# Kernel tuning notes

Hardware: AMD Instinct MI355X
Metric: run time of the kernel (lower is better)

The kernel has to match this reference:

```python
import jax, jax.numpy as jnp
import numpy as np

ALPHA = 1.0   # alpha=1 -> loss = alpha*loss_shape; temporal term weighted by (1-alpha)=0
GAMMA = 0.01  # soft-DTW smoothing
G = 0.05      # logistic weight steepness (weighted-DTW, Jeong et al. 2011)
BIG = 1e9     # finite 'infinity' (keeps vjp NaN-free vs. true inf)


def _softdtw(D, gamma):
    # Soft-DTW value of cost matrix D [N,N] via anti-diagonal (wavefront) scan.
    # R(i,j) = D[i,j] + softmin_gamma(R(i-1,j-1), R(i-1,j), R(i,j-1)),
    # R(-1,-1)=0, other out-of-range = +inf. Diagonal k holds cells (i, k-i).
    N = D.shape[-1]
    i = jnp.arange(N)

    def step(carry, k):
        r2, r1 = carry            # diagonals k-2 and k-1, indexed by row i
        j = k - i
        valid = (j >= 0) & (j < N)
        dk = jnp.where(valid, D[i, jnp.clip(j, 0, N - 1)], 0.0)
        up = jnp.where(i > 0, jnp.roll(r1, 1), BIG)     # R(i-1, j)
        left = r1                                        # R(i, j-1) (BIG where invalid)
        dg = jnp.where(i > 0, jnp.roll(r2, 1), BIG)      # R(i-1, j-1)
        dg = jnp.where((i == 0) & (j == 0), 0.0, dg)     # R(-1,-1) = 0 boundary
        smin = -gamma * jax.nn.logsumexp(jnp.stack([-dg, -up, -left]) / gamma, axis=0)
        rk = jnp.where(valid, dk + smin, BIG)
        return (r1, rk), None

    r0 = jnp.full((N,), BIG, dtype=D.dtype)
    (_, rlast), _ = jax.lax.scan(step, (r0, r0), jnp.arange(2 * N - 1))
    return rlast[N - 1]  # cell (N-1, N-1)


def _weighted_dilate(inp, tgt):
    B, N, _ = inp.shape
    idx = jnp.arange(N, dtype=inp.dtype)
    # modified-logistic weight on |i-j|, midpoint N/2, steepness g
    w = 1.0 / (1.0 + jnp.exp(-G * (jnp.abs(idx[:, None] - idx[None, :]) - N / 2.0)))
    # pairwise squared euclidean cost: D[b,i,j] = sum_d (tgt[b,i,d]-inp[b,j,d])^2
    D = jnp.sum((tgt[:, :, None, :] - inp[:, None, :, :]) ** 2, axis=-1) * w
    sdtw = jax.vmap(lambda d: _softdtw(d, GAMMA))(D)  # [B]
    loss_shape = jnp.mean(sdtw)
    return ALPHA * loss_shape  # (1-alpha)*loss_temporal == 0 at default alpha=1


def setup_inputs() -> dict:
    key = jax.random.key(0)
    k1, k2 = jax.random.split(key)
    B, N, Dm = 32, 1024, 1
    return {
        "input": jax.random.normal(k1, (B, N, Dm), dtype=jnp.float32),
        "target": jax.random.normal(k2, (B, N, Dm), dtype=jnp.float32),
    }


def reference(input, target):
    return _weighted_dilate(input, target)
```

## Files before the change

kernel.cpp:

```cpp
#include <hip/hip_runtime.h>
#include <math.h>

#define NN 1024
#define BATCH 32
#define P 8
#define NW 4
#define THREADS 256
#define DD 32
#define SW 32
#define SPAN 160
#define NT 64
#define RB 2
#define GW 0.05f
#define K2 144.2695040888963f
#define INV_K2 0.0069314718055994531f
#define BIGS 1.4426950408889634e11f

#define EXP2F(x) __builtin_amdgcn_exp2f(x)
#define LOG2F(x) __builtin_amdgcn_logf(x)

typedef unsigned long long u64;

__device__ __forceinline__ float dppshr(float oldv, float src) {
    return __int_as_float(__builtin_amdgcn_update_dpp(
        __float_as_int(oldv), __float_as_int(src), 0x138, 0xF, 0xF, false));
}

__device__ __forceinline__ u64 pk(float v, unsigned tag) {
    return ((u64)tag << 32) | (u64)__float_as_uint(v);
}

__global__ __launch_bounds__(256) void ws_init(int* __restrict__ acks,
                                               u64* __restrict__ gx) {
    if (blockIdx.x == 128) acks[threadIdx.x] = 0;
    else gx[(size_t)blockIdx.x * 256 + threadIdx.x] = 0;
}

__global__ __launch_bounds__(THREADS) void sdtw_pipe8(
        const float* __restrict__ inp, const float* __restrict__ tgt,
        float* __restrict__ partial, int* __restrict__ acks,
        u64* __restrict__ gx)
{
    __shared__ float xs[NN];
    __shared__ float wlblk[3136];
    __shared__ float2 exch[2][SPAN];

    const int bid = blockIdx.x;
    const int b = bid & 31;
    const int p = bid >> 5;
    const int tid = threadIdx.x;
    const int w = tid >> 6;
    const int lane = tid & 63;

    for (int tdx = tid; tdx < NN; tdx += THREADS) {
        xs[tdx] = inp[b * NN + tdx];
        float mO = (float)(2 * tdx + 1) - 1023.0f;
        float mE = (float)(2 * tdx) - 1023.0f;
        wlblk[544 + tdx]        = K2 / (1.0f + __expf(-GW * (fabsf(mO) - 512.0f)));
        wlblk[544 + 1024 + tdx] = K2 / (1.0f + __expf(-GW * (fabsf(mE) - 512.0f)));
    }

    const int i = 128 * p - (DD - 1) + SW * w + lane;
    const int i0 = i - lane;
    const bool rowValid = (unsigned)i < (unsigned)NN;
    int ic = min(max(i, 0), NN - 1);
    const float ti = tgt[b * NN + ic];
    const int imask = rowValid ? i : 0x3FFFFFFF;
    const float* wpBase = &wlblk[544 + 511 - i];

    float r1 = BIGS, r2 = BIGS;
    float dgp = (i == 0) ? 0.0f : BIGS;
    float bndUp = BIGS;
    float xv = 0.0f;
    int ackC = 0;

    __syncthreads();

    const int fin = b * P + p;
    const int fout = fin + 1;
    u64* gout = gx + (size_t)fout * (RB * DD * 2);
    u64* ginb = gx + (size_t)fin * (RB * DD * 2);

    const bool isProd = (w == NW - 1) && (p < P - 1);
    const bool isCons = (w == 0) && (p > 0);

    u64 pfA = 0, pfB = 0, pfC0 = 0, pfC1 = 0;

    for (int t = 0; t < NT; ++t) {
        if (t > 0) {
            if (isProd) {
                if (t > RB) {
                    while (ackC < t - RB) {
                        __builtin_amdgcn_s_sleep(1);
                        ackC = __hip_atomic_load(&acks[fout], __ATOMIC_RELAXED,
                                                 __HIP_MEMORY_SCOPE_AGENT);
                    }
                }
                if (lane >= DD - 1 && lane < 63) {
                    u64* gq = gout + (size_t)((t - 1) & (RB - 1)) * (DD * 2)
                                   + (size_t)(lane - (DD - 1)) * 2;
                    __hip_atomic_store(&gq[0], pk(r1, (unsigned)t),
                                       __ATOMIC_RELAXED, __HIP_MEMORY_SCOPE_AGENT);
                    __hip_atomic_store(&gq[1], pk(r2, (unsigned)t),
                                       __ATOMIC_RELAXED, __HIP_MEMORY_SCOPE_AGENT);
                }
                ackC = __hip_atomic_load(&acks[fout], __ATOMIC_RELAXED,
                                         __HIP_MEMORY_SCOPE_AGENT);
            }
            if (w > 0) {
                const int buf = (t - 1) & 1;
                if (lane < DD - 1) { float2 v = exch[buf][SW * w + lane]; r1 = v.x; r2 = v.y; }
                float2 bv = exch[buf][SW * w - 1];
                float nd = dppshr(0.0f, r2);
                if (lane == 0)           { bndUp = bv.x; dgp = bv.y; }
                else if (lane <= DD - 2) dgp = nd;
            } else if (p > 0) {
                const unsigned expect = (unsigned)t;
                const u64* gslot = ginb + (size_t)((t - 1) & (RB - 1)) * (DD * 2);
                for (;;) {
                    int ok = 1;
                    if (lane < DD - 1)
                        ok = ((unsigned)(pfA >> 32) == expect) &
                             ((unsigned)(pfB >> 32) == expect);
                    if (lane == 0)
                        ok &= ((unsigned)(pfC0 >> 32) == expect) &
                              ((unsigned)(pfC1 >> 32) == expect);
                    if (__all(ok)) break;
                    if (lane < DD - 1) {
                        pfA = __hip_atomic_load((u64*)&gslot[(size_t)(lane + 1) * 2],
                                                __ATOMIC_RELAXED, __HIP_MEMORY_SCOPE_AGENT);
                        pfB = __hip_atomic_load((u64*)&gslot[(size_t)(lane + 1) * 2 + 1],
                                                __ATOMIC_RELAXED, __HIP_MEMORY_SCOPE_AGENT);
                    }
                    if (lane == 0) {
                        pfC0 = __hip_atomic_load((u64*)&gslot[0],
                                                 __ATOMIC_RELAXED, __HIP_MEMORY_SCOPE_AGENT);
                        pfC1 = __hip_atomic_load((u64*)&gslot[1],
                                                 __ATOMIC_RELAXED, __HIP_MEMORY_SCOPE_AGENT);
                    }
                }
                if (lane < DD - 1) { r1 = __uint_as_float((unsigned)pfA);
                                     r2 = __uint_as_float((unsigned)pfB); }
                float nd = dppshr(0.0f, r2);
                if (lane == 0) { bndUp = __uint_as_float((unsigned)pfC0);
                                 dgp   = __uint_as_float((unsigned)pfC1); }
                else if (lane <= DD - 2) dgp = nd;
                if (lane == 0)
                    __hip_atomic_store(&acks[fin], (int)(pfC0 >> 32),
                                       __ATOMIC_RELAXED, __HIP_MEMORY_SCOPE_AGENT);
            } else {
                bndUp = BIGS;
            }
        }

        const int kbase = t << 5;
        const float* wp = wpBase + (t << 4);
        int c = kbase - 1 - i;  c = min(max(c, 0), NN - 1);
        xv = xs[c];
        int c0 = kbase - i0;    c0 = min(max(c0, 0), NN - 1);
        const float xf0 = xs[c0];
        const int jj0 = kbase - imask;

        #pragma unroll
        for (int d = 0; d < DD; ++d) {
            xv = dppshr((d == 0) ? xf0 : xv, xv);
            const float up = dppshr((d == 0) ? bndUp : r1, r1);
            const float dg = dgp;
            const float left = r1;
            const float wv = (d & 1) ? wp[1024 + ((d + 1) >> 1)]
                                     : wp[(d >> 1)];
            const float diff = ti - xv;
            const float dk = diff * diff * wv;
            const float mn = fminf(fminf(dg, up), left);
            const float md = __builtin_amdgcn_fmed3f(dg, up, left);
            const float mx = fmaxf(fmaxf(dg, up), left);
            const float s = 1.0f + EXP2F(mn - md) + EXP2F(mn - mx);
            float r = dk + mn - LOG2F(s);
            r = (jj0 >= -d) ? r : BIGS;
            r2 = r1; r1 = r; dgp = up;
        }
        if (t == NT - 1) break;

        if (w < NW - 1 && lane >= DD - 1)
            exch[t & 1][SW * w + lane] = make_float2(r1, r2);

        if (isCons) {
            const u64* gslot = ginb + (size_t)(t & (RB - 1)) * (DD * 2);
            if (lane < DD - 1) {
                pfA = __hip_atomic_load((u64*)&gslot[(size_t)(lane + 1) * 2],
                                        __ATOMIC_RELAXED, __HIP_MEMORY_SCOPE_AGENT);
                pfB = __hip_atomic_load((u64*)&gslot[(size_t)(lane + 1) * 2 + 1],
                                        __ATOMIC_RELAXED, __HIP_MEMORY_SCOPE_AGENT);
            }
            if (lane == 0) {
                pfC0 = __hip_atomic_load((u64*)&gslot[0],
                                         __ATOMIC_RELAXED, __HIP_MEMORY_SCOPE_AGENT);
                pfC1 = __hip_atomic_load((u64*)&gslot[1],
                                         __ATOMIC_RELAXED, __HIP_MEMORY_SCOPE_AGENT);
            }
        }

        asm volatile("s_waitcnt lgkmcnt(0)" ::: "memory");
        __builtin_amdgcn_s_barrier();
        asm volatile("" ::: "memory");
        __builtin_amdgcn_sched_barrier(0);
    }

    if (i == NN - 1) partial[b] = r2 * INV_K2;
}

__global__ __launch_bounds__(64) void reduce_mean32(const float* __restrict__ partial,
                                                    float* __restrict__ out) {
    float v = (threadIdx.x < BATCH) ? partial[threadIdx.x] : 0.0f;
    #pragma unroll
    for (int off = 32; off > 0; off >>= 1) v += __shfl_down(v, off);
    if (threadIdx.x == 0) out[0] = v * (1.0f / (float)BATCH);
}

extern "C" void kernel_launch(void* const* d_in, const int* in_sizes, int n_in,
                              void* d_out, int out_size, void* d_ws, size_t ws_size,
                              hipStream_t stream) {
    const float* inp = (const float*)d_in[0];
    const float* tgt = (const float*)d_in[1];
    float* out = (float*)d_out;

    float* partial = (float*)d_ws;
    int* acks  = (int*)((char*)d_ws + 128);
    u64* gx    = (u64*)((char*)d_ws + 2048);

    ws_init<<<129, 256, 0, stream>>>(acks, gx);
    sdtw_pipe8<<<BATCH * P, THREADS, 0, stream>>>(inp, tgt, partial, acks, gx);
    reduce_mean32<<<1, 64, 0, stream>>>(partial, out);
}
```

Baseline: 216.7 us.

## Pack two batch elements per block with 512 threads and shared weight table

Each workgroup now handles two batch elements, using eight wavefronts in two groups of four, so the grid halves from 256 to 128 blocks. Both sequences share the logistic-weight table, which halves its redundant computation, and the intra-block exchange buffers are duplicated per sequence. The risk is that the __syncthreads now spans two independent pipelines, and fewer blocks means fewer CUs are used. Two batch items per CU compete for issue slots in a latency-bound recurrence.

```diff
diff --git a/kernel.cpp b/kernel.cpp
--- a/kernel.cpp
+++ b/kernel.cpp
@@ -4,8 +4,10 @@
 #define NN 1024
 #define BATCH 32
 #define P 8
+#define NB 2
+#define PAIRS 16
 #define NW 4
-#define THREADS 256
+#define THREADS 512
 #define DD 32
 #define SW 32
 #define SPAN 160
@@ -41,26 +43,33 @@
         float* __restrict__ partial, int* __restrict__ acks,
         u64* __restrict__ gx)
 {
-    __shared__ float xs[NN];
+    __shared__ float xs[NB][NN];
     __shared__ float wlblk[3136];
-    __shared__ float2 exch[2][SPAN];
+    __shared__ float2 exch[NB][2][SPAN];
 
     const int bid = blockIdx.x;
-    const int b = bid & 31;
-    const int p = bid >> 5;
+    const int pair = bid & 15;
+    const int p = bid >> 4;
     const int tid = threadIdx.x;
     const int w = tid >> 6;
+    const int s = w >> 2;
+    const int v = w & 3;
     const int lane = tid & 63;
-
+    const int b = pair * NB + s;
+
+    const int b0 = pair * NB;
     for (int tdx = tid; tdx < NN; tdx += THREADS) {
-        xs[tdx] = inp[b * NN + tdx];
+        xs[0][tdx] = inp[b0 * NN + tdx];
+        xs[1][tdx] = inp[(b0 + 1) * NN + tdx];
         float mO = (float)(2 * tdx + 1) - 1023.0f;
         float mE = (float)(2 * tdx) - 1023.0f;
         wlblk[544 + tdx]        = K2 / (1.0f + __expf(-GW * (fabsf(mO) - 512.0f)));
         wlblk[544 + 1024 + tdx] = K2 / (1.0f + __expf(-GW * (fabsf(mE) - 512.0f)));
     }
 
-    const int i = 128 * p - (DD - 1) + SW * w + lane;
+    const float* xsb = xs[s];
+
+    const int i = 128 * p - (DD - 1) + SW * v + lane;
     const int i0 = i - lane;
     const bool rowValid = (unsigned)i < (unsigned)NN;
     int ic = min(max(i, 0), NN - 1);
@@ -81,8 +90,8 @@
     u64* gout = gx + (size_t)fout * (RB * DD * 2);
     u64* ginb = gx + (size_t)fin * (RB * DD * 2);
 
-    const bool isProd = (w == NW - 1) && (p < P - 1);
-    const bool isCons = (w == 0) && (p > 0);
+    const bool isProd = (v == NW - 1) && (p < P - 1);
+    const bool isCons = (v == 0) && (p > 0);
 
     u64 pfA = 0, pfB = 0, pfC0 = 0, pfC1 = 0;
 
@@ -107,10 +116,10 @@
                 ackC = __hip_atomic_load(&acks[fout], __ATOMIC_RELAXED,
                                          __HIP_MEMORY_SCOPE_AGENT);
             }
-            if (w > 0) {
+            if (v > 0) {
                 const int buf = (t - 1) & 1;
-                if (lane < DD - 1) { float2 v = exch[buf][SW * w + lane]; r1 = v.x; r2 = v.y; }
-                float2 bv = exch[buf][SW * w - 1];
+                if (lane < DD - 1) { float2 vv = exch[s][buf][SW * v + lane]; r1 = vv.x; r2 = vv.y; }
+                float2 bv = exch[s][buf][SW * v - 1];
                 float nd = dppshr(0.0f, r2);
                 if (lane == 0)           { bndUp = bv.x; dgp = bv.y; }
                 else if (lane <= DD - 2) dgp = nd;
@@ -156,9 +165,9 @@
         const int kbase = t << 5;
         const float* wp = wpBase + (t << 4);
         int c = kbase - 1 - i;  c = min(max(c, 0), NN - 1);
-        xv = xs[c];
+        xv = xsb[c];
         int c0 = kbase - i0;    c0 = min(max(c0, 0), NN - 1);
-        const float xf0 = xs[c0];
+        const float xf0 = xsb[c0];
         const int jj0 = kbase - imask;
 
         #pragma unroll
@@ -174,15 +183,15 @@
             const float mn = fminf(fminf(dg, up), left);
             const float md = __builtin_amdgcn_fmed3f(dg, up, left);
             const float mx = fmaxf(fmaxf(dg, up), left);
-            const float s = 1.0f + EXP2F(mn - md) + EXP2F(mn - mx);
-            float r = dk + mn - LOG2F(s);
+            const float ss = 1.0f + EXP2F(mn - md) + EXP2F(mn - mx);
+            float r = dk + mn - LOG2F(ss);
             r = (jj0 >= -d) ? r : BIGS;
             r2 = r1; r1 = r; dgp = up;
         }
         if (t == NT - 1) break;
 
-        if (w < NW - 1 && lane >= DD - 1)
-            exch[t & 1][SW * w + lane] = make_float2(r1, r2);
+        if (v < NW - 1 && lane >= DD - 1)
+            exch[s][t & 1][SW * v + lane] = make_float2(r1, r2);
 
         if (isCons) {
             const u64* gslot = ginb + (size_t)(t & (RB - 1)) * (DD * 2);
@@ -229,6 +238,6 @@
     u64* gx    = (u64*)((char*)d_ws + 2048);
 
     ws_init<<<129, 256, 0, stream>>>(acks, gx);
-    sdtw_pipe8<<<BATCH * P, THREADS, 0, stream>>>(inp, tgt, partial, acks, gx);
+    sdtw_pipe8<<<PAIRS * P, THREADS, 0, stream>>>(inp, tgt, partial, acks, gx);
     reduce_mean32<<<1, 64, 0, stream>>>(partial, out);
 }
```

Result: slower. 270.6 us (+24.8%).

## Vectorize weight loads, prefetch x values, and skip masking in interior tiles

Applied to the files above, without the earlier changes.

Rebuilds the weight table as a per-block contiguous window so each thread loads its 32 weights with float2 reads into registers before the step loop, replacing 32 scalar LDS reads. It prefetches the next tile's x-values one iteration early to hide LDS latency, and adds an unmasked fast path for tiles that lie entirely inside the valid region. The cost is higher register pressure from the wreg array and doubled code size from the two unrolled loop variants.

```diff
diff --git a/kernel.cpp b/kernel.cpp
--- a/kernel.cpp
+++ b/kernel.cpp
@@ -11,6 +11,7 @@
 #define SPAN 160
 #define NT 64
 #define RB 2
+#define WLN 2368
 #define GW 0.05f
 #define K2 144.2695040888963f
 #define INV_K2 0.0069314718055994531f
@@ -35,14 +36,30 @@
     if (blockIdx.x == 128) acks[threadIdx.x] = 0;
     else gx[(size_t)blockIdx.x * 256 + threadIdx.x] = 0;
 }
+
+#define STEPBODY(d, DOMASK) do {                                              \
+        xv = dppshr(((d) == 0) ? xf0 : xv, xv);        \
+        const float up = dppshr(((d) == 0) ? bndUp : r1, r1);  \
+        const float dg = dgp;                                                 \
+        const float left = r1;                                                \
+        const float diff = ti - xv;                                           \
+        const float dk = diff * diff * wreg[(d)];         \
+        const float mn = fminf(fminf(dg, up), left);                          \
+        const float md = __builtin_amdgcn_fmed3f(dg, up, left);               \
+        const float mx = fmaxf(fmaxf(dg, up), left);                          \
+        const float ss = 1.0f + EXP2F(mn - md) + EXP2F(mn - mx);              \
+        float r = dk + mn - LOG2F(ss);                                        \
+        if (DOMASK) r = (jj0 >= -(d)) ? r : BIGS;        \
+        r2 = r1; r1 = r; dgp = up;                                            \
+    } while (0)
 
 __global__ __launch_bounds__(THREADS) void sdtw_pipe8(
         const float* __restrict__ inp, const float* __restrict__ tgt,
         float* __restrict__ partial, int* __restrict__ acks,
         u64* __restrict__ gx)
 {
-    __shared__ float xs[NN];
-    __shared__ float wlblk[3136];
+    __shared__ __align__(16) float xs[NN];
+    __shared__ __align__(16) float wlu[WLN];
     __shared__ float2 exch[2][SPAN];
 
     const int bid = blockIdx.x;
@@ -52,12 +69,15 @@
     const int w = tid >> 6;
     const int lane = tid & 63;
 
-    for (int tdx = tid; tdx < NN; tdx += THREADS) {
+    const int mlo = 767 - 256 * p;
+    for (int tdx = tid; tdx < NN; tdx += THREADS)
         xs[tdx] = inp[b * NN + tdx];
-        float mO = (float)(2 * tdx + 1) - 1023.0f;
-        float mE = (float)(2 * tdx) - 1023.0f;
-        wlblk[544 + tdx]        = K2 / (1.0f + __expf(-GW * (fabsf(mO) - 512.0f)));
-        wlblk[544 + 1024 + tdx] = K2 / (1.0f + __expf(-GW * (fabsf(mE) - 512.0f)));
+    for (int tdx = tid; tdx < WLN; tdx += THREADS) {
+        int m = tdx + mlo;
+        float val = K2;
+        if ((unsigned)m <= 2046u)
+            val = K2 / (1.0f + __expf(-GW * (fabsf((float)m - 1023.0f) - 512.0f)));
+        wlu[tdx] = val;
     }
 
     const int i = 128 * p - (DD - 1) + SW * w + lane;
@@ -66,7 +86,7 @@
     int ic = min(max(i, 0), NN - 1);
     const float ti = tgt[b * NN + ic];
     const int imask = rowValid ? i : 0x3FFFFFFF;
-    const float* wpBase = &wlblk[544 + 511 - i];
+    const int wq = 256 + 256 * p - 2 * i;
 
     float r1 = BIGS, r2 = BIGS;
     float dgp = (i == 0) ? 0.0f : BIGS;
@@ -85,6 +105,11 @@
     const bool isCons = (w == 0) && (p > 0);
 
     u64 pfA = 0, pfB = 0, pfC0 = 0, pfC1 = 0;
+
+    int cP  = min(max(-1 - i, 0), NN - 1);
+    int c0P = min(max(-i0, 0), NN - 1);
+    float xpreA = xs[cP];
+    float xpreB = xs[c0P];
 
     for (int t = 0; t < NT; ++t) {
         if (t > 0) {
@@ -109,7 +134,7 @@
             }
             if (w > 0) {
                 const int buf = (t - 1) & 1;
-                if (lane < DD - 1) { float2 v = exch[buf][SW * w + lane]; r1 = v.x; r2 = v.y; }
+                if (lane < DD - 1) { float2 vv = exch[buf][SW * w + lane]; r1 = vv.x; r2 = vv.y; }
                 float2 bv = exch[buf][SW * w - 1];
                 float nd = dppshr(0.0f, r2);
                 if (lane == 0)           { bndUp = bv.x; dgp = bv.y; }
@@ -154,30 +179,28 @@
         }
 
         const int kbase = t << 5;
-        const float* wp = wpBase + (t << 4);
-        int c = kbase - 1 - i;  c = min(max(c, 0), NN - 1);
-        xv = xs[c];
-        int c0 = kbase - i0;    c0 = min(max(c0, 0), NN - 1);
-        const float xf0 = xs[c0];
         const int jj0 = kbase - imask;
 
+        const float* wp = &wlu[kbase + wq];
+        float wreg[DD];
         #pragma unroll
-        for (int d = 0; d < DD; ++d) {
-            xv = dppshr((d == 0) ? xf0 : xv, xv);
-            const float up = dppshr((d == 0) ? bndUp : r1, r1);
-            const float dg = dgp;
-            const float left = r1;
-            const float wv = (d & 1) ? wp[1024 + ((d + 1) >> 1)]
-                                     : wp[(d >> 1)];
-            const float diff = ti - xv;
-            const float dk = diff * diff * wv;
-            const float mn = fminf(fminf(dg, up), left);
-            const float md = __builtin_amdgcn_fmed3f(dg, up, left);
-            const float mx = fmaxf(fmaxf(dg, up), left);
-            const float s = 1.0f + EXP2F(mn - md) + EXP2F(mn - mx);
-            float r = dk + mn - LOG2F(s);
-            r = (jj0 >= -d) ? r : BIGS;
-            r2 = r1; r1 = r; dgp = up;
+        for (int h = 0; h < DD / 2; ++h) {
+            float2 w2 = *reinterpret_cast<const float2*>(&wp[2 * h]);
+            wreg[2 * h] = w2.x; wreg[2 * h + 1] = w2.y;
+        }
+
+        const float xf0 = xpreB;
+        xv = xpreA;
+        { int cN  = min(max(kbase + DD - 1 - i, 0), NN - 1);
+          int c0N = min(max(kbase + DD - i0, 0), NN - 1);
+          xpreA = xs[cN]; xpreB = xs[c0N]; }
+
+        if (i0 >= 0 && kbase >= i0 + 63) {
+            #pragma unroll
+            for (int d = 0; d < DD; ++d) STEPBODY(d, 0);
+        } else {
+            #pragma unroll
+            for (int d = 0; d < DD; ++d) STEPBODY(d, 1);
         }
         if (t == NT - 1) break;
 
```

After: 205.3 us. 5.3% less time.
